# Performance work log

Measured on AMD Instinct MI355X. Metric: run time of the kernel, lower is better.

The kernel has to match this reference:

```python
import jax, jax.numpy as jnp
import numpy as np

B, S, D, H = 4, 2048, 1024, 16
HD = D // H


def sinusoidal_pe(max_len, d_model):
    pos = np.arange(max_len)[:, None].astype(np.float32)
    div = np.exp(np.arange(0, d_model, 2).astype(np.float32) * (-np.log(10000.0) / d_model))
    pe = np.zeros((max_len, d_model), dtype=np.float32)
    pe[:, 0::2] = np.sin(pos * div)
    pe[:, 1::2] = np.cos(pos * div)
    return jnp.asarray(pe)


def setup_inputs() -> dict:
    key = jax.random.key(0)
    ks = jax.random.split(key, 9)
    s = 1.0 / np.sqrt(D)
    inp = {
        "x": jax.random.normal(ks[0], (B, S, D), dtype=jnp.float32),
        "Wq": jax.random.normal(ks[1], (D, D), dtype=jnp.float32) * s,
        "bq": jnp.zeros((D,), dtype=jnp.float32),
        "Wk": jax.random.normal(ks[2], (D, D), dtype=jnp.float32) * s,
        "bk": jnp.zeros((D,), dtype=jnp.float32),
        "Wv": jax.random.normal(ks[3], (D, D), dtype=jnp.float32) * s,
        "bv": jnp.zeros((D,), dtype=jnp.float32),
        "Wp": jax.random.normal(ks[4], (D, D), dtype=jnp.float32) * s,
        "bp": jnp.zeros((D,), dtype=jnp.float32),
        "pe": sinusoidal_pe(S, D),
    }
    return inp


def reference(x, Wq, bq, Wk, bk, Wv, bv, Wp, bp, pe):
    # positional encoding (eval mode: dropout is identity)
    xp = x + pe[None, :, :]  # [B,S,D]
    split = lambda t: t.reshape(B, S, H, HD).transpose(0, 2, 1, 3)  # [B,H,S,HD]
    q = split(xp @ Wq.T + bq)
    k = split(xp @ Wk.T + bk)
    v = split(xp @ Wv.T + bv)
    scores = jnp.einsum("bhqd,bhkd->bhqk", q, k) / jnp.sqrt(jnp.float32(HD))
    attn = jax.nn.softmax(scores, axis=-1)
    ctx = jnp.einsum("bhqk,bhkd->bhqd", attn, v)
    ctx = ctx.transpose(0, 2, 1, 3).reshape(B, S, D)
    return ctx @ Wp.T + bp
```

## Files before the change

### kernel.cpp

```cpp
#include <hip/hip_runtime.h>
#include <hip/hip_bf16.h>
#include <stdint.h>

#define B_  4
#define S_  2048
#define D_  1024
#define H_  16
#define HD_ 64

typedef __bf16 bfx8   __attribute__((ext_vector_type(8)));
typedef float  f32x4  __attribute__((ext_vector_type(4)));
typedef float  f32x16 __attribute__((ext_vector_type(16)));
typedef short  s16x4  __attribute__((ext_vector_type(4)));
typedef short  s16x8  __attribute__((ext_vector_type(8)));
typedef float  fl4    __attribute__((ext_vector_type(4)));
typedef unsigned int u32x2 __attribute__((ext_vector_type(2)));
typedef unsigned int u32x4 __attribute__((ext_vector_type(4)));

#define EXP2(x) __builtin_amdgcn_exp2f(x)

static __device__ __forceinline__ unsigned short f2bf(float f) {
    union { float f; unsigned int u; } v; v.f = f;
    unsigned int r = v.u + 0x7fffu + ((v.u >> 16) & 1u);
    return (unsigned short)(r >> 16);
}
static __device__ __forceinline__ unsigned int fbits(float f) {
    union { float f; unsigned int u; } v; v.f = f; return v.u;
}

#define GLD_LDS16(gp, lp) __builtin_amdgcn_global_load_lds( \
    (const __attribute__((address_space(1))) unsigned int*)(gp), \
    (__attribute__((address_space(3))) unsigned int*)(lp), 16, 0, 0)

__global__ __launch_bounds__(256) void prep_kernel(
    const float* __restrict__ x, const float* __restrict__ pe,
    const float* __restrict__ w0, const float* __restrict__ w1,
    const float* __restrict__ w2, const float* __restrict__ w3,
    unsigned short* __restrict__ xpb, unsigned short* __restrict__ wcat)
{
    const int blk = blockIdx.x;
    if (blk < 4096) {
        int i = (blk * 256 + threadIdx.x) * 8;
        fl4 xv0 = *(const fl4*)(x + i);
        fl4 xv1 = *(const fl4*)(x + i + 4);
        fl4 pv0 = *(const fl4*)(pe + (i & (S_ * D_ - 1)));
        fl4 pv1 = *(const fl4*)(pe + ((i + 4) & (S_ * D_ - 1)));
        s16x8 r;
#pragma unroll
        for (int j = 0; j < 4; j++) r[j]     = (short)f2bf(xv0[j] + pv0[j]);
#pragma unroll
        for (int j = 0; j < 4; j++) r[4 + j] = (short)f2bf(xv1[j] + pv1[j]);
        *(s16x8*)(xpb + i) = r;
    } else {
        const int bb = blk - 4096;
        const int wsel = bb >> 9;
        const float* src = wsel == 0 ? w0 : wsel == 1 ? w1 : wsel == 2 ? w2 : w3;
        int i = (((bb & 511) * 256) + threadIdx.x) * 8;
        fl4 v0 = *(const fl4*)(src + i);
        fl4 v1 = *(const fl4*)(src + i + 4);
        s16x8 r;
#pragma unroll
        for (int j = 0; j < 4; j++) r[j]     = (short)f2bf(v0[j]);
#pragma unroll
        for (int j = 0; j < 4; j++) r[4 + j] = (short)f2bf(v1[j]);
        *(s16x8*)(wcat + (size_t)wsel * D_ * D_ + i) = r;
    }
}

#define RD64(buf, row, ks, lg) \
    (*(const bfx8*)((buf) + (row) * 64 + ((((ks) * 4 + (lg)) ^ ((row) & 7)) * 8)))

__global__ __launch_bounds__(256, 2) void gemm_qkv(
    const unsigned short* __restrict__ A,
    const unsigned short* __restrict__ Bw,
    const float* __restrict__ bq, const float* __restrict__ bk,
    const float* __restrict__ bv,
    unsigned short* __restrict__ Qo, unsigned short* __restrict__ Ko,
    unsigned short* __restrict__ Vo, float qscale)
{
    constexpr int K = D_;
    __shared__ __align__(16) unsigned short As[2][128 * 64];
    __shared__ __align__(16) unsigned short Bs[2][128 * 64];
    const int hw  = blockIdx.x;
    const int xcd = hw & 7;
    const int i_  = hw >> 3;
    const int m0  = (i_ / 3) * 128;
    const int n0  = (xcd * 3 + i_ % 3) * 128;

    const int t  = threadIdx.x;
    const int l  = t & 63;
    const int w  = t >> 6;
    const int wr = (w >> 1) * 64;
    const int wc = (w & 1) * 64;
    const int lr = l & 15;
    const int lg = l >> 4;

    const int sr = t >> 3;
    const int sc = (((t & 7) ^ (sr & 7)) * 8);
    const unsigned short* pA = A  + (size_t)(m0 + sr) * K + sc;
    const unsigned short* pB = Bw + (size_t)(n0 + sr) * K + sc;
    const int e0 = t * 8;

#define STAGE64(dst, p, kofs) do {                                   \
    GLD_LDS16((p) + (kofs),                        (dst) + e0);      \
    GLD_LDS16((p) + (kofs) + (size_t)32 * K,       (dst) + 2048 + e0); \
    GLD_LDS16((p) + (kofs) + (size_t)64 * K,       (dst) + 4096 + e0); \
    GLD_LDS16((p) + (kofs) + (size_t)96 * K,       (dst) + 6144 + e0); \
} while (0)

    f32x4 acc[4][4] = {};

    STAGE64(As[0], pA, 0);
    STAGE64(Bs[0], pB, 0);
    __syncthreads();

    int cur = 0;
    for (int k0 = 0; k0 < K; k0 += 64) {
        if (k0 + 64 < K) {
            STAGE64(As[cur ^ 1], pA, k0 + 64);
            STAGE64(Bs[cur ^ 1], pB, k0 + 64);
        }
        const unsigned short* Ac = As[cur];
        const unsigned short* Bc = Bs[cur];
#pragma unroll
        for (int ks = 0; ks < 2; ks++) {
            bfx8 af[4], bf[4];
#pragma unroll
            for (int i = 0; i < 4; i++)
                af[i] = RD64(Ac, wr + i * 16 + lr, ks, lg);
#pragma unroll
            for (int i = 0; i < 4; i++)
                bf[i] = RD64(Bc, wc + i * 16 + lr, ks, lg);
#pragma unroll
            for (int i = 0; i < 4; i++)
#pragma unroll
                for (int j = 0; j < 4; j++)
                    acc[i][j] = __builtin_amdgcn_mfma_f32_16x16x32_bf16(
                        af[i], bf[j], acc[i][j], 0, 0, 0);
        }
        __syncthreads();
        cur ^= 1;
    }

    const int sel = n0 >> 10;
    const float* bias = sel == 0 ? bq : sel == 1 ? bk : bv;
    const float osc = sel == 0 ? qscale : 1.0f;

#pragma unroll
    for (int i = 0; i < 4; i++) {
        const int row0 = m0 + wr + i * 16 + lg * 4;
#pragma unroll
        for (int j = 0; j < 4; j++) {
            const int colf = n0 + wc + j * 16 + lr;
            const int ocol = colf & 1023;
            const float bvv = bias[ocol];
            if (sel < 2) {
                unsigned short* C = sel == 0 ? Qo : Ko;
#pragma unroll
                for (int v = 0; v < 4; v++)
                    C[(size_t)(row0 + v) * D_ + ocol] = f2bf((acc[i][j][v] + bvv) * osc);
            } else {
                const int bidx = row0 >> 11;
                const int s0   = row0 & (S_ - 1);
                s16x4 r;
#pragma unroll
                for (int v = 0; v < 4; v++) r[v] = (short)f2bf(acc[i][j][v] + bvv);
                *(s16x4*)(Vo + (size_t)(bidx * D_ + ocol) * S_ + s0) = r;
            }
        }
    }
#undef STAGE64
}

__global__ __launch_bounds__(256, 2) void gemm_out(
    const unsigned short* __restrict__ A,
    const unsigned short* __restrict__ Bw,
    const float* __restrict__ bias,
    float* __restrict__ Cout)
{
    constexpr int K = D_;
    constexpr int N = D_;
    __shared__ __align__(16) unsigned short As[2][128 * 64];
    __shared__ __align__(16) unsigned short Bs[2][128 * 64];
    const int hw = blockIdx.x;
    const int logical = (hw & 7) * 64 + (hw >> 3);
    const int m0 = (logical >> 3) * 128;
    const int n0 = (logical & 7) * 128;

    const int t  = threadIdx.x;
    const int l  = t & 63;
    const int w  = t >> 6;
    const int wr = (w >> 1) * 64;
    const int wc = (w & 1) * 64;
    const int lr = l & 15;
    const int lg = l >> 4;

    const int sr = t >> 3;
    const int sc = (((t & 7) ^ (sr & 7)) * 8);
    const unsigned short* pA = A  + (size_t)(m0 + sr) * K + sc;
    const unsigned short* pB = Bw + (size_t)(n0 + sr) * K + sc;
    const int e0 = t * 8;

#define STAGE64(dst, p, kofs) do {                                   \
    GLD_LDS16((p) + (kofs),                        (dst) + e0);      \
    GLD_LDS16((p) + (kofs) + (size_t)32 * K,       (dst) + 2048 + e0); \
    GLD_LDS16((p) + (kofs) + (size_t)64 * K,       (dst) + 4096 + e0); \
    GLD_LDS16((p) + (kofs) + (size_t)96 * K,       (dst) + 6144 + e0); \
} while (0)

    f32x4 acc[4][4] = {};

    STAGE64(As[0], pA, 0);
    STAGE64(Bs[0], pB, 0);
    __syncthreads();

    int cur = 0;
    for (int k0 = 0; k0 < K; k0 += 64) {
        if (k0 + 64 < K) {
            STAGE64(As[cur ^ 1], pA, k0 + 64);
            STAGE64(Bs[cur ^ 1], pB, k0 + 64);
        }
        const unsigned short* Ac = As[cur];
        const unsigned short* Bc = Bs[cur];
#pragma unroll
        for (int ks = 0; ks < 2; ks++) {
            bfx8 af[4], bf[4];
#pragma unroll
            for (int i = 0; i < 4; i++)
                af[i] = RD64(Ac, wr + i * 16 + lr, ks, lg);
#pragma unroll
            for (int i = 0; i < 4; i++)
                bf[i] = RD64(Bc, wc + i * 16 + lr, ks, lg);
#pragma unroll
            for (int i = 0; i < 4; i++)
#pragma unroll
                for (int j = 0; j < 4; j++)
                    acc[i][j] = __builtin_amdgcn_mfma_f32_16x16x32_bf16(
                        af[i], bf[j], acc[i][j], 0, 0, 0);
        }
        __syncthreads();
        cur ^= 1;
    }

#pragma unroll
    for (int i = 0; i < 4; i++) {
        const int row0 = m0 + wr + i * 16 + lg * 4;
#pragma unroll
        for (int j = 0; j < 4; j++) {
            const int col = n0 + wc + j * 16 + lr;
            const float bv = bias[col];
#pragma unroll
            for (int v = 0; v < 4; v++)
                Cout[(size_t)(row0 + v) * N + col] = acc[i][j][v] + bv;
        }
    }
#undef STAGE64
}

__global__ __launch_bounds__(512, 4) void attn_kernel(
    const unsigned short* __restrict__ Qb,
    const unsigned short* __restrict__ Kb,
    const unsigned short* __restrict__ Vt,
    unsigned short* __restrict__ Ctx)
{
    __shared__ __align__(16) unsigned short Ks[2][32 * 128];
    __shared__ __align__(16) unsigned short Vs[2][32 * 128];

    const int hw = blockIdx.x;
    const int logical = (hw & 7) * 64 + (hw >> 3);
    const int bh = logical >> 3;
    const int t  = threadIdx.x;
    const int l  = t & 63;
    const int w  = t >> 6;
    const int b  = bh >> 4;
    const int h  = bh & 15;
    const int lr = l & 31;
    const int hi = l >> 5;
    const int q0 = (logical & 7) * 256 + w * 32;

    const unsigned short* Qbase = Qb + (size_t)b * S_ * D_ + h * HD_;
    const unsigned short* Kbase = Kb + (size_t)b * S_ * D_ + h * HD_;
    const unsigned short* Vbase = Vt + (size_t)bh * HD_ * S_;

    const int jrow = t >> 4;
    const int c16  = (t & 15) ^ (jrow & 15);
    const int r0   = (c16 >> 3) * 32 + jrow;
    const int cc8  = (c16 & 7) * 8;
    const unsigned short* Ksrc = Kbase + (size_t)r0 * D_ + cc8;
    const unsigned short* Vsrc = Vbase + (size_t)r0 * S_ + cc8;
    const int ld = t * 8;

    GLD_LDS16(Ksrc, &Ks[0][ld]);
    GLD_LDS16(Vsrc, &Vs[0][ld]);

    bfx8 qf[4];
#pragma unroll
    for (int t4 = 0; t4 < 4; t4++)
        qf[t4] = *(const bfx8*)(Qbase + (size_t)(q0 + lr) * D_ + t4 * 16 + hi * 8);

    f32x16 acc0 = {}, acc1 = {};
    float l_r = 0.f;
    const int sw16 = lr & 15;

#define FRD(buf, half, cs) \
    (*(const bfx8*)((buf) + lr * 128 + ((((half) * 8 + (cs)) ^ sw16) * 8)))

    int cur = 0;
    for (int ki = 0; ki < S_ / 64; ki++) {
        __syncthreads();
        if (ki + 1 < S_ / 64) {
            GLD_LDS16(Ksrc + (size_t)(ki + 1) * 64 * D_, &Ks[cur ^ 1][ld]);
            GLD_LDS16(Vsrc + (ki + 1) * 64,              &Vs[cur ^ 1][ld]);
        }
        const unsigned short* Kc = Ks[cur];
        const unsigned short* Vc = Vs[cur];

        f32x16 s0 = {}, s1 = {};
        __builtin_amdgcn_s_setprio(1);
#pragma unroll
        for (int t4 = 0; t4 < 4; t4++) {
            bfx8 a0 = FRD(Kc, 0, t4 * 2 + hi);
            bfx8 a1 = FRD(Kc, 1, t4 * 2 + hi);
            s0 = __builtin_amdgcn_mfma_f32_32x32x16_bf16(a0, qf[t4], s0, 0, 0, 0);
            s1 = __builtin_amdgcn_mfma_f32_32x32x16_bf16(a1, qf[t4], s1, 0, 0, 0);
        }
        __builtin_amdgcn_s_setprio(0);

        float c0 = 0.f, c1 = 0.f, c2 = 0.f, c3 = 0.f;
#pragma unroll
        for (int r = 0; r < 16; r += 4) {
            float p0 = EXP2(s0[r]);     s0[r] = p0;     c0 += p0;
            float p1 = EXP2(s0[r + 1]); s0[r + 1] = p1; c1 += p1;
            float p2 = EXP2(s0[r + 2]); s0[r + 2] = p2; c2 += p2;
            float p3 = EXP2(s0[r + 3]); s0[r + 3] = p3; c3 += p3;
        }
#pragma unroll
        for (int r = 0; r < 16; r += 4) {
            float p0 = EXP2(s1[r]);     s1[r] = p0;     c0 += p0;
            float p1 = EXP2(s1[r + 1]); s1[r + 1] = p1; c1 += p1;
            float p2 = EXP2(s1[r + 2]); s1[r + 2] = p2; c2 += p2;
            float p3 = EXP2(s1[r + 3]); s1[r + 3] = p3; c3 += p3;
        }
        l_r += (c0 + c1) + (c2 + c3);

        unsigned pk0[8], pk1[8];
#pragma unroll
        for (int i = 0; i < 8; i++) {
            pk0[i] = __builtin_amdgcn_perm(fbits(s0[2 * i + 1]), fbits(s0[2 * i]), 0x07060302u);
            pk1[i] = __builtin_amdgcn_perm(fbits(s1[2 * i + 1]), fbits(s1[2 * i]), 0x07060302u);
        }

#pragma unroll
        for (int ks = 0; ks < 4; ks++) {
            const int c = (ks & 1) * 4;
            const unsigned pa0 = (ks >> 1) ? pk1[c]     : pk0[c];
            const unsigned pa1 = (ks >> 1) ? pk1[c + 1] : pk0[c + 1];
            const unsigned pa2 = (ks >> 1) ? pk1[c + 2] : pk0[c + 2];
            const unsigned pa3 = (ks >> 1) ? pk1[c + 3] : pk0[c + 3];
            u32x2 r02 = __builtin_amdgcn_permlane32_swap(pa0, pa2, false, false);
            u32x2 r13 = __builtin_amdgcn_permlane32_swap(pa1, pa3, false, false);
            u32x4 bfr;
            bfr[0] = r02[0];
            bfr[1] = r13[0];
            bfr[2] = r02[1];
            bfr[3] = r13[1];
            union { u32x4 u; bfx8 b; } cvt; cvt.u = bfr;

            bfx8 v0 = FRD(Vc, 0, ks * 2 + hi);
            bfx8 v1 = FRD(Vc, 1, ks * 2 + hi);
            __builtin_amdgcn_s_setprio(1);
            acc0 = __builtin_amdgcn_mfma_f32_32x32x16_bf16(v0, cvt.b, acc0, 0, 0, 0);
            acc1 = __builtin_amdgcn_mfma_f32_32x32x16_bf16(v1, cvt.b, acc1, 0, 0, 0);
            __builtin_amdgcn_s_setprio(0);
        }
        cur ^= 1;
    }
#undef FRD

    const float l_tot = l_r + __shfl_xor(l_r, 32);
    const float rinv = 1.0f / l_tot;
    unsigned short* Cb = Ctx + (size_t)b * S_ * D_ + (size_t)(q0 + lr) * D_ + h * HD_;
#pragma unroll
    for (int dt = 0; dt < 2; dt++)
#pragma unroll
        for (int a = 0; a < 4; a++) {
            s16x4 rv;
#pragma unroll
            for (int v = 0; v < 4; v++)
                rv[v] = (short)f2bf((dt ? acc1[4 * a + v] : acc0[4 * a + v]) * rinv);
            *(s16x4*)(Cb + dt * 32 + 8 * a + 4 * hi) = rv;
        }
}

extern "C" void kernel_launch(void* const* d_in, const int* in_sizes, int n_in,
                              void* d_out, int out_size, void* d_ws, size_t ws_size,
                              hipStream_t stream)
{
    const float* x  = (const float*)d_in[0];
    const float* Wq = (const float*)d_in[1];
    const float* bq = (const float*)d_in[2];
    const float* Wk = (const float*)d_in[3];
    const float* bk = (const float*)d_in[4];
    const float* Wv = (const float*)d_in[5];
    const float* bv = (const float*)d_in[6];
    const float* Wp = (const float*)d_in[7];
    const float* bp = (const float*)d_in[8];
    const float* pe = (const float*)d_in[9];

    char* ws = (char*)d_ws;
    const size_t MD = (size_t)B_ * S_ * D_;
    unsigned short* xpb = (unsigned short*)ws; ws += MD * 2;
    unsigned short* wqb = (unsigned short*)ws; ws += (size_t)D_ * D_ * 2;
    unsigned short* wkb = (unsigned short*)ws; ws += (size_t)D_ * D_ * 2;
    unsigned short* wvb = (unsigned short*)ws; ws += (size_t)D_ * D_ * 2;
    unsigned short* wpb = (unsigned short*)ws; ws += (size_t)D_ * D_ * 2;
    unsigned short* qb  = (unsigned short*)ws; ws += MD * 2;
    unsigned short* kb  = (unsigned short*)ws; ws += MD * 2;
    unsigned short* vtb = (unsigned short*)ws; ws += MD * 2;
    unsigned short* ctb = (unsigned short*)ws; ws += MD * 2;

    prep_kernel<<<6144, 256, 0, stream>>>(x, pe, Wq, Wk, Wv, Wp, xpb, wqb);

    const float qscale = 0.125f * 1.44269504088896340736f;

    gemm_qkv<<<1536, 256, 0, stream>>>(xpb, wqb, bq, bk, bv, qb, kb, vtb, qscale);

    attn_kernel<<<512, 512, 0, stream>>>(qb, kb, vtb, ctb);

    gemm_out<<<512, 256, 0, stream>>>(ctb, wpb, bp, (float*)d_out);
}
```

Baseline: 181.7 us.

## Replace both GEMMs with an 8-wave 128x256 triple-buffered pipelined GEMM template

The separate QKV and output-projection GEMMs are merged into one templated kernel. It uses 512 threads with a 128x256 output tile, a three-stage LDS ring filled by direct global-to-LDS loads, and explicit vmcnt/lgkmcnt waits and barriers. The B-tile loads are split across two half-iterations so they overlap the MFMA phases, and MFMA sections run at raised wave priority. The aim is better data reuse per block and better overlap of loads with compute. In exchange it allows only one block per CU, uses about 144KB of LDS, and depends on hand-counted wait counts that must stay correct.

```diff
diff --git a/kernel.cpp b/kernel.cpp
--- a/kernel.cpp
+++ b/kernel.cpp
@@ -31,6 +31,8 @@
 #define GLD_LDS16(gp, lp) __builtin_amdgcn_global_load_lds( \
     (const __attribute__((address_space(1))) unsigned int*)(gp), \
     (__attribute__((address_space(3))) unsigned int*)(lp), 16, 0, 0)
+
+#define MFMA16(a, b, c) __builtin_amdgcn_mfma_f32_16x16x32_bf16((a), (b), (c), 0, 0, 0)
 
 __global__ __launch_bounds__(256) void prep_kernel(
     const float* __restrict__ x, const float* __restrict__ pe,
@@ -70,28 +72,31 @@
 #define RD64(buf, row, ks, lg) \
     (*(const bfx8*)((buf) + (row) * 64 + ((((ks) * 4 + (lg)) ^ ((row) & 7)) * 8)))
 
-__global__ __launch_bounds__(256, 2) void gemm_qkv(
+template<int MODE>
+__global__ __launch_bounds__(512, 1) void gemm_8w(
     const unsigned short* __restrict__ A,
     const unsigned short* __restrict__ Bw,
-    const float* __restrict__ bq, const float* __restrict__ bk,
-    const float* __restrict__ bv,
-    unsigned short* __restrict__ Qo, unsigned short* __restrict__ Ko,
-    unsigned short* __restrict__ Vo, float qscale)
+    const float* __restrict__ b0, const float* __restrict__ b1,
+    const float* __restrict__ b2,
+    unsigned short* __restrict__ O0, unsigned short* __restrict__ O1,
+    unsigned short* __restrict__ O2, float* __restrict__ Fo, float qscale)
 {
-    constexpr int K = D_;
-    __shared__ __align__(16) unsigned short As[2][128 * 64];
-    __shared__ __align__(16) unsigned short Bs[2][128 * 64];
+    constexpr int K   = D_;
+    constexpr int NKT = 16;
+    __shared__ __align__(16) unsigned short As[3][128 * 64];
+    __shared__ __align__(16) unsigned short Bs[3][256 * 64];
+
     const int hw  = blockIdx.x;
     const int xcd = hw & 7;
     const int i_  = hw >> 3;
-    const int m0  = (i_ / 3) * 128;
-    const int n0  = (xcd * 3 + i_ % 3) * 128;
+    const int m0  = (xcd * 8 + (i_ & 7)) * 128;
+    const int n0  = (i_ >> 3) * 256;
 
     const int t  = threadIdx.x;
+    const int w  = t >> 6;
+    const int wm = (w >> 2) * 64;
+    const int wn = (w & 3) * 64;
     const int l  = t & 63;
-    const int w  = t >> 6;
-    const int wr = (w >> 1) * 64;
-    const int wc = (w & 1) * 64;
     const int lr = l & 15;
     const int lg = l >> 4;
 
@@ -101,160 +106,134 @@
     const unsigned short* pB = Bw + (size_t)(n0 + sr) * K + sc;
     const int e0 = t * 8;
 
-#define STAGE64(dst, p, kofs) do {                                   \
-    GLD_LDS16((p) + (kofs),                        (dst) + e0);      \
-    GLD_LDS16((p) + (kofs) + (size_t)32 * K,       (dst) + 2048 + e0); \
-    GLD_LDS16((p) + (kofs) + (size_t)64 * K,       (dst) + 4096 + e0); \
-    GLD_LDS16((p) + (kofs) + (size_t)96 * K,       (dst) + 6144 + e0); \
+#define STAGE_A(dst, kofs) do {                                        \
+    GLD_LDS16(pA + (kofs),                   (dst) + e0);              \
+    GLD_LDS16(pA + (kofs) + (size_t)64 * K,  (dst) + 4096 + e0);       \
 } while (0)
+#define STAGE_B1(dst, kofs, kk) \
+    GLD_LDS16(pB + (kofs) + (size_t)(kk) * 64 * K, (dst) + (kk) * 4096 + e0)
 
     f32x4 acc[4][4] = {};
-
-    STAGE64(As[0], pA, 0);
-    STAGE64(Bs[0], pB, 0);
-    __syncthreads();
-
-    int cur = 0;
-    for (int k0 = 0; k0 < K; k0 += 64) {
-        if (k0 + 64 < K) {
-            STAGE64(As[cur ^ 1], pA, k0 + 64);
-            STAGE64(Bs[cur ^ 1], pB, k0 + 64);
-        }
-        const unsigned short* Ac = As[cur];
-        const unsigned short* Bc = Bs[cur];
-#pragma unroll
-        for (int ks = 0; ks < 2; ks++) {
-            bfx8 af[4], bf[4];
-#pragma unroll
-            for (int i = 0; i < 4; i++)
-                af[i] = RD64(Ac, wr + i * 16 + lr, ks, lg);
-#pragma unroll
-            for (int i = 0; i < 4; i++)
-                bf[i] = RD64(Bc, wc + i * 16 + lr, ks, lg);
-#pragma unroll
-            for (int i = 0; i < 4; i++)
-#pragma unroll
-                for (int j = 0; j < 4; j++)
-                    acc[i][j] = __builtin_amdgcn_mfma_f32_16x16x32_bf16(
-                        af[i], bf[j], acc[i][j], 0, 0, 0);
-        }
-        __syncthreads();
-        cur ^= 1;
+    bfx8 af[4][2], bfa[2][2], bfb[2][2];
+
+    STAGE_A(As[0], 0);
+    STAGE_B1(Bs[0], 0, 0); STAGE_B1(Bs[0], 0, 1);
+    STAGE_B1(Bs[0], 0, 2); STAGE_B1(Bs[0], 0, 3);
+    STAGE_A(As[1], 64);
+    STAGE_B1(Bs[1], 64, 0); STAGE_B1(Bs[1], 64, 1);
+    STAGE_B1(Bs[1], 64, 2); STAGE_B1(Bs[1], 64, 3);
+    asm volatile("s_waitcnt vmcnt(6)" ::: "memory");
+    __builtin_amdgcn_sched_barrier(0);
+    __builtin_amdgcn_s_barrier();
+
+    int c = 0, c2 = 2;
+    for (int kt = 0; kt < NKT; ++kt) {
+        const unsigned short* Ac = As[c];
+        const unsigned short* Bc = Bs[c];
+        unsigned short* An = As[c2];
+        unsigned short* Bn = Bs[c2];
+        const int kn = (kt + 2) * 64;
+        const bool st = (kt + 2) < NKT;
+
+#pragma unroll
+        for (int i = 0; i < 4; i++) {
+            af[i][0] = RD64(Ac, wm + i * 16 + lr, 0, lg);
+            af[i][1] = RD64(Ac, wm + i * 16 + lr, 1, lg);
+        }
+#pragma unroll
+        for (int j = 0; j < 2; j++) {
+            bfa[j][0] = RD64(Bc, wn + j * 16 + lr, 0, lg);
+            bfa[j][1] = RD64(Bc, wn + j * 16 + lr, 1, lg);
+        }
+        if (st) { STAGE_A(An, kn); STAGE_B1(Bn, kn, 0); }
+        __builtin_amdgcn_s_barrier();
+        asm volatile("s_waitcnt lgkmcnt(0)" ::: "memory");
+        __builtin_amdgcn_sched_barrier(0);
+        __builtin_amdgcn_s_setprio(1);
+#pragma unroll
+        for (int i = 0; i < 4; i++)
+#pragma unroll
+            for (int j = 0; j < 2; j++) {
+                acc[i][j] = MFMA16(af[i][0], bfa[j][0], acc[i][j]);
+                acc[i][j] = MFMA16(af[i][1], bfa[j][1], acc[i][j]);
+            }
+        __builtin_amdgcn_s_setprio(0);
+        __builtin_amdgcn_sched_barrier(0);
+        __builtin_amdgcn_s_barrier();
+
+#pragma unroll
+        for (int j = 0; j < 2; j++) {
+            bfb[j][0] = RD64(Bc, wn + 32 + j * 16 + lr, 0, lg);
+            bfb[j][1] = RD64(Bc, wn + 32 + j * 16 + lr, 1, lg);
+        }
+        if (st) { STAGE_B1(Bn, kn, 1); STAGE_B1(Bn, kn, 2); STAGE_B1(Bn, kn, 3); }
+        if (kt < NKT - 2)
+            asm volatile("s_waitcnt vmcnt(6)" ::: "memory");
+        else
+            asm volatile("s_waitcnt vmcnt(0)" ::: "memory");
+        __builtin_amdgcn_sched_barrier(0);
+        __builtin_amdgcn_s_barrier();
+        asm volatile("s_waitcnt lgkmcnt(0)" ::: "memory");
+        __builtin_amdgcn_sched_barrier(0);
+        __builtin_amdgcn_s_setprio(1);
+#pragma unroll
+        for (int i = 0; i < 4; i++)
+#pragma unroll
+            for (int j = 0; j < 2; j++) {
+                acc[i][2 + j] = MFMA16(af[i][0], bfb[j][0], acc[i][2 + j]);
+                acc[i][2 + j] = MFMA16(af[i][1], bfb[j][1], acc[i][2 + j]);
+            }
+        __builtin_amdgcn_s_setprio(0);
+        __builtin_amdgcn_sched_barrier(0);
+        __builtin_amdgcn_s_barrier();
+
+        c  = (c  == 2) ? 0 : c + 1;
+        c2 = (c2 == 2) ? 0 : c2 + 1;
     }
 
-    const int sel = n0 >> 10;
-    const float* bias = sel == 0 ? bq : sel == 1 ? bk : bv;
-    const float osc = sel == 0 ? qscale : 1.0f;
-
-#pragma unroll
-    for (int i = 0; i < 4; i++) {
-        const int row0 = m0 + wr + i * 16 + lg * 4;
-#pragma unroll
-        for (int j = 0; j < 4; j++) {
-            const int colf = n0 + wc + j * 16 + lr;
-            const int ocol = colf & 1023;
-            const float bvv = bias[ocol];
-            if (sel < 2) {
-                unsigned short* C = sel == 0 ? Qo : Ko;
+    if (MODE == 0) {
+        const int sel = n0 >> 10;
+        const float* bias = sel == 0 ? b0 : sel == 1 ? b1 : b2;
+        const float osc = sel == 0 ? qscale : 1.0f;
+#pragma unroll
+        for (int i = 0; i < 4; i++) {
+            const int row0 = m0 + wm + i * 16 + lg * 4;
+#pragma unroll
+            for (int j = 0; j < 4; j++) {
+                const int colf = n0 + wn + j * 16 + lr;
+                const int ocol = colf & 1023;
+                const float bvv = bias[ocol];
+                if (sel < 2) {
+                    unsigned short* C = sel == 0 ? O0 : O1;
+#pragma unroll
+                    for (int v = 0; v < 4; v++)
+                        C[(size_t)(row0 + v) * D_ + ocol] = f2bf((acc[i][j][v] + bvv) * osc);
+                } else {
+                    const int bidx = row0 >> 11;
+                    const int s0   = row0 & (S_ - 1);
+                    s16x4 r;
+#pragma unroll
+                    for (int v = 0; v < 4; v++) r[v] = (short)f2bf(acc[i][j][v] + bvv);
+                    *(s16x4*)(O2 + (size_t)(bidx * D_ + ocol) * S_ + s0) = r;
+                }
+            }
+        }
+    } else {
+#pragma unroll
+        for (int i = 0; i < 4; i++) {
+            const int row0 = m0 + wm + i * 16 + lg * 4;
+#pragma unroll
+            for (int j = 0; j < 4; j++) {
+                const int col = n0 + wn + j * 16 + lr;
+                const float bvv = b0[col];
 #pragma unroll
                 for (int v = 0; v < 4; v++)
-                    C[(size_t)(row0 + v) * D_ + ocol] = f2bf((acc[i][j][v] + bvv) * osc);
-            } else {
-                const int bidx = row0 >> 11;
-                const int s0   = row0 & (S_ - 1);
-                s16x4 r;
-#pragma unroll
-                for (int v = 0; v < 4; v++) r[v] = (short)f2bf(acc[i][j][v] + bvv);
-                *(s16x4*)(Vo + (size_t)(bidx * D_ + ocol) * S_ + s0) = r;
+                    Fo[(size_t)(row0 + v) * D_ + col] = acc[i][j][v] + bvv;
             }
         }
     }
-#undef STAGE64
-}
-
-__global__ __launch_bounds__(256, 2) void gemm_out(
-    const unsigned short* __restrict__ A,
-    const unsigned short* __restrict__ Bw,
-    const float* __restrict__ bias,
-    float* __restrict__ Cout)
-{
-    constexpr int K = D_;
-    constexpr int N = D_;
-    __shared__ __align__(16) unsigned short As[2][128 * 64];
-    __shared__ __align__(16) unsigned short Bs[2][128 * 64];
-    const int hw = blockIdx.x;
-    const int logical = (hw & 7) * 64 + (hw >> 3);
-    const int m0 = (logical >> 3) * 128;
-    const int n0 = (logical & 7) * 128;
-
-    const int t  = threadIdx.x;
-    const int l  = t & 63;
-    const int w  = t >> 6;
-    const int wr = (w >> 1) * 64;
-    const int wc = (w & 1) * 64;
-    const int lr = l & 15;
-    const int lg = l >> 4;
-
-    const int sr = t >> 3;
-    const int sc = (((t & 7) ^ (sr & 7)) * 8);
-    const unsigned short* pA = A  + (size_t)(m0 + sr) * K + sc;
-    const unsigned short* pB = Bw + (size_t)(n0 + sr) * K + sc;
-    const int e0 = t * 8;
-
-#define STAGE64(dst, p, kofs) do {                                   \
-    GLD_LDS16((p) + (kofs),                        (dst) + e0);      \
-    GLD_LDS16((p) + (kofs) + (size_t)32 * K,       (dst) + 2048 + e0); \
-    GLD_LDS16((p) + (kofs) + (size_t)64 * K,       (dst) + 4096 + e0); \
-    GLD_LDS16((p) + (kofs) + (size_t)96 * K,       (dst) + 6144 + e0); \
-} while (0)
-
-    f32x4 acc[4][4] = {};
-
-    STAGE64(As[0], pA, 0);
-    STAGE64(Bs[0], pB, 0);
-    __syncthreads();
-
-    int cur = 0;
-    for (int k0 = 0; k0 < K; k0 += 64) {
-        if (k0 + 64 < K) {
-            STAGE64(As[cur ^ 1], pA, k0 + 64);
-            STAGE64(Bs[cur ^ 1], pB, k0 + 64);
-        }
-        const unsigned short* Ac = As[cur];
-        const unsigned short* Bc = Bs[cur];
-#pragma unroll
-        for (int ks = 0; ks < 2; ks++) {
-            bfx8 af[4], bf[4];
-#pragma unroll
-            for (int i = 0; i < 4; i++)
-                af[i] = RD64(Ac, wr + i * 16 + lr, ks, lg);
-#pragma unroll
-            for (int i = 0; i < 4; i++)
-                bf[i] = RD64(Bc, wc + i * 16 + lr, ks, lg);
-#pragma unroll
-            for (int i = 0; i < 4; i++)
-#pragma unroll
-                for (int j = 0; j < 4; j++)
-                    acc[i][j] = __builtin_amdgcn_mfma_f32_16x16x32_bf16(
-                        af[i], bf[j], acc[i][j], 0, 0, 0);
-        }
-        __syncthreads();
-        cur ^= 1;
-    }
-
-#pragma unroll
-    for (int i = 0; i < 4; i++) {
-        const int row0 = m0 + wr + i * 16 + lg * 4;
-#pragma unroll
-        for (int j = 0; j < 4; j++) {
-            const int col = n0 + wc + j * 16 + lr;
-            const float bv = bias[col];
-#pragma unroll
-            for (int v = 0; v < 4; v++)
-                Cout[(size_t)(row0 + v) * N + col] = acc[i][j][v] + bv;
-        }
-    }
-#undef STAGE64
+#undef STAGE_A
+#undef STAGE_B1
 }
 
 __global__ __launch_bounds__(512, 4) void attn_kernel(
@@ -423,9 +402,11 @@
 
     const float qscale = 0.125f * 1.44269504088896340736f;
 
-    gemm_qkv<<<1536, 256, 0, stream>>>(xpb, wqb, bq, bk, bv, qb, kb, vtb, qscale);
+    gemm_8w<0><<<768, 512, 0, stream>>>(xpb, wqb, bq, bk, bv,
+                                        qb, kb, vtb, nullptr, qscale);
 
     attn_kernel<<<512, 512, 0, stream>>>(qb, kb, vtb, ctb);
 
-    gemm_out<<<512, 256, 0, stream>>>(ctb, wpb, bp, (float*)d_out);
-}
+    gemm_8w<1><<<256, 512, 0, stream>>>(ctb, wpb, bp, nullptr, nullptr,
+                                        nullptr, nullptr, nullptr, (float*)d_out, 1.0f);
+}
```

Measured after the change: 184.8 us. About the same (+1.7%).

## Split attention over two key halves with a separate combine kernel

Applied to the files above, without the earlier changes.

The attention kernel is split so each block processes only half of the keys (16 tiles instead of 32), which doubles the grid to 1024 blocks. Each block writes unnormalized bf16 partial outputs plus its row sums. A new combine kernel adds the two partials and divides by the total sum. This is meant to improve CU occupancy and load balance, at the cost of an extra launch, extra global traffic for the partial buffers, and an extra bf16 rounding of the partials. The merge is only correct if both halves share the same exponent reference.

```diff
diff --git a/kernel.cpp b/kernel.cpp
--- a/kernel.cpp
+++ b/kernel.cpp
@@ -26,6 +26,9 @@
 }
 static __device__ __forceinline__ unsigned int fbits(float f) {
     union { float f; unsigned int u; } v; v.f = f; return v.u;
+}
+static __device__ __forceinline__ float bf2f(unsigned short s) {
+    union { unsigned int u; float f; } v; v.u = ((unsigned int)s) << 16; return v.f;
 }
 
 #define GLD_LDS16(gp, lp) __builtin_amdgcn_global_load_lds( \
@@ -257,18 +260,21 @@
 #undef STAGE64
 }
 
-__global__ __launch_bounds__(512, 4) void attn_kernel(
+__global__ __launch_bounds__(512, 8) void attn_split(
     const unsigned short* __restrict__ Qb,
     const unsigned short* __restrict__ Kb,
     const unsigned short* __restrict__ Vt,
-    unsigned short* __restrict__ Ctx)
+    unsigned short* __restrict__ Op,
+    float* __restrict__ Lp)
 {
     __shared__ __align__(16) unsigned short Ks[2][32 * 128];
     __shared__ __align__(16) unsigned short Vs[2][32 * 128];
 
     const int hw = blockIdx.x;
-    const int logical = (hw & 7) * 64 + (hw >> 3);
-    const int bh = logical >> 3;
+    const int logical = (hw & 7) * 128 + (hw >> 3);
+    const int qt   = logical & 7;
+    const int part = (logical >> 3) & 1;
+    const int bh   = logical >> 4;
     const int t  = threadIdx.x;
     const int l  = t & 63;
     const int w  = t >> 6;
@@ -276,7 +282,7 @@
     const int h  = bh & 15;
     const int lr = l & 31;
     const int hi = l >> 5;
-    const int q0 = (logical & 7) * 256 + w * 32;
+    const int q0 = qt * 256 + w * 32;
 
     const unsigned short* Qbase = Qb + (size_t)b * S_ * D_ + h * HD_;
     const unsigned short* Kbase = Kb + (size_t)b * S_ * D_ + h * HD_;
@@ -286,8 +292,8 @@
     const int c16  = (t & 15) ^ (jrow & 15);
     const int r0   = (c16 >> 3) * 32 + jrow;
     const int cc8  = (c16 & 7) * 8;
-    const unsigned short* Ksrc = Kbase + (size_t)r0 * D_ + cc8;
-    const unsigned short* Vsrc = Vbase + (size_t)r0 * S_ + cc8;
+    const unsigned short* Ksrc = Kbase + (size_t)(r0 + part * 1024) * D_ + cc8;
+    const unsigned short* Vsrc = Vbase + (size_t)r0 * S_ + part * 1024 + cc8;
     const int ld = t * 8;
 
     GLD_LDS16(Ksrc, &Ks[0][ld]);
@@ -306,9 +312,9 @@
     (*(const bfx8*)((buf) + lr * 128 + ((((half) * 8 + (cs)) ^ sw16) * 8)))
 
     int cur = 0;
-    for (int ki = 0; ki < S_ / 64; ki++) {
+    for (int ki = 0; ki < 16; ki++) {
         __syncthreads();
-        if (ki + 1 < S_ / 64) {
+        if (ki + 1 < 16) {
             GLD_LDS16(Ksrc + (size_t)(ki + 1) * 64 * D_, &Ks[cur ^ 1][ld]);
             GLD_LDS16(Vsrc + (ki + 1) * 64,              &Vs[cur ^ 1][ld]);
         }
@@ -378,8 +384,8 @@
 #undef FRD
 
     const float l_tot = l_r + __shfl_xor(l_r, 32);
-    const float rinv = 1.0f / l_tot;
-    unsigned short* Cb = Ctx + (size_t)b * S_ * D_ + (size_t)(q0 + lr) * D_ + h * HD_;
+    unsigned short* Ob = Op + (size_t)part * (B_ * S_ * D_)
+                       + (size_t)(b * S_ + q0 + lr) * D_ + h * HD_;
 #pragma unroll
     for (int dt = 0; dt < 2; dt++)
 #pragma unroll
@@ -387,9 +393,34 @@
             s16x4 rv;
 #pragma unroll
             for (int v = 0; v < 4; v++)
-                rv[v] = (short)f2bf((dt ? acc1[4 * a + v] : acc0[4 * a + v]) * rinv);
-            *(s16x4*)(Cb + dt * 32 + 8 * a + 4 * hi) = rv;
-        }
+                rv[v] = (short)f2bf(dt ? acc1[4 * a + v] : acc0[4 * a + v]);
+            *(s16x4*)(Ob + dt * 32 + 8 * a + 4 * hi) = rv;
+        }
+    if (hi == 0)
+        Lp[(size_t)((part * B_ + b) * H_ + h) * S_ + q0 + lr] = l_tot;
+}
+
+__global__ __launch_bounds__(256) void combine_kernel(
+    const unsigned short* __restrict__ Op, const float* __restrict__ Lp,
+    unsigned short* __restrict__ ctb)
+{
+    const size_t MD = (size_t)B_ * S_ * D_;
+    const int i = (blockIdx.x * 256 + threadIdx.x) * 8;
+    const int col = i & 1023;
+    const int h   = col >> 6;
+    const int bq  = i >> 10;
+    const int b   = bq >> 11;
+    const int q   = bq & (S_ - 1);
+    const float l0 = Lp[(size_t)(b * H_ + h) * S_ + q];
+    const float l1 = Lp[(size_t)((B_ + b) * H_ + h) * S_ + q];
+    const float rinv = 1.0f / (l0 + l1);
+    s16x8 o0 = *(const s16x8*)(Op + i);
+    s16x8 o1 = *(const s16x8*)(Op + MD + i);
+    s16x8 r;
+#pragma unroll
+    for (int j = 0; j < 8; j++)
+        r[j] = (short)f2bf((bf2f((unsigned short)o0[j]) + bf2f((unsigned short)o1[j])) * rinv);
+    *(s16x8*)(ctb + i) = r;
 }
 
 extern "C" void kernel_launch(void* const* d_in, const int* in_sizes, int n_in,
@@ -418,6 +449,14 @@
     unsigned short* kb  = (unsigned short*)ws; ws += MD * 2;
     unsigned short* vtb = (unsigned short*)ws; ws += MD * 2;
     unsigned short* ctb = (unsigned short*)ws; ws += MD * 2;
+    unsigned short* op1 = (unsigned short*)ws; ws += MD * 2;
+    float*          lp  = (float*)ws;          ws += (size_t)2 * B_ * H_ * S_ * 4;
+
+
+    unsigned short* opar = op1;
+    unsigned short* part1 = (unsigned short*)((char*)op1 + MD * 2);
+    (void)part1;
+    lp = (float*)((char*)op1 + MD * 2 * 2);
 
     prep_kernel<<<6144, 256, 0, stream>>>(x, pe, Wq, Wk, Wv, Wp, xpb, wqb);
 
@@ -425,7 +464,9 @@
 
     gemm_qkv<<<1536, 256, 0, stream>>>(xpb, wqb, bq, bk, bv, qb, kb, vtb, qscale);
 
-    attn_kernel<<<512, 512, 0, stream>>>(qb, kb, vtb, ctb);
+    attn_split<<<1024, 512, 0, stream>>>(qb, kb, vtb, opar, lp);
+
+    combine_kernel<<<(int)(MD / (256 * 8)), 256, 0, stream>>>(opar, lp, ctb);
 
     gemm_out<<<512, 256, 0, stream>>>(ctb, wpb, bp, (float*)d_out);
 }
```

New measurement: 706.3 us. +288.7%, slower.
